# Performance work log

Measured on AMD Instinct MI355X. Metric: run time of the kernel, lower is better.

The kernel has to match this reference:

```python
import jax, jax.numpy as jnp
import numpy as np

D_MODEL = 1024
H = 16
D_HEAD = D_MODEL // H


def setup_inputs() -> dict:
    key = jax.random.key(0)
    ks = jax.random.split(key, 9)
    B, S = 2, 2048
    x = jax.random.normal(ks[0], (B, S, D_MODEL), dtype=jnp.float32)
    s = 1.0 / np.sqrt(D_HEAD)
    # per-head Q/K/V linears, stacked: W[h, out, in], b[h, out] (torch Linear: y = x W^T + b)
    Wq = jax.random.normal(ks[1], (H, D_HEAD, D_HEAD), dtype=jnp.float32) * s
    bq = jax.random.normal(ks[2], (H, D_HEAD), dtype=jnp.float32) * 0.01
    Wk = jax.random.normal(ks[3], (H, D_HEAD, D_HEAD), dtype=jnp.float32) * s
    bk = jax.random.normal(ks[4], (H, D_HEAD), dtype=jnp.float32) * 0.01
    Wv = jax.random.normal(ks[5], (H, D_HEAD, D_HEAD), dtype=jnp.float32) * s
    bv = jax.random.normal(ks[6], (H, D_HEAD), dtype=jnp.float32) * 0.01
    Wo = jax.random.normal(ks[7], (D_MODEL, D_MODEL), dtype=jnp.float32) / np.sqrt(D_MODEL)
    bo = jax.random.normal(ks[8], (D_MODEL,), dtype=jnp.float32) * 0.01
    return {"x": x, "Wq": Wq, "bq": bq, "Wk": Wk, "bk": bk,
            "Wv": Wv, "bv": bv, "Wo": Wo, "bo": bo}


def reference(x, Wq, bq, Wk, bk, Wv, bv, Wo, bo):
    B, S, D = x.shape
    xh = x.reshape(B, S, H, D_HEAD)  # split along feature dim, head-major
    q = jnp.einsum('bshi,hoi->bsho', xh, Wq) + bq
    k = jnp.einsum('bshi,hoi->bsho', xh, Wk) + bk
    v = jnp.einsum('bshi,hoi->bsho', xh, Wv) + bv
    scale = 1.0 / jnp.sqrt(jnp.asarray(D_HEAD, dtype=x.dtype))  # source scales by sqrt(d_model//h)
    scores = jnp.einsum('bqhd,bkhd->bhqk', q, k) * scale
    causal = jnp.tril(jnp.ones((S, S), dtype=bool))
    scores = jnp.where(causal, scores, -jnp.inf)
    attn = jax.nn.softmax(scores, axis=-1)
    out = jnp.einsum('bhqk,bkhd->bqhd', attn, v).reshape(B, S, D)
    return out @ Wo.T + bo
```

## Files before the change

kernel.cpp:

```cpp
#include <hip/hip_runtime.h>
#include <cstddef>

#define Bc 2
#define Sc 2048
#define Dc 1024
#define Hc 16
#define QSC 0.18033688011112042f

typedef short short8 __attribute__((ext_vector_type(8)));
typedef float floatx4 __attribute__((ext_vector_type(4)));
typedef unsigned short ushort_t;

#if __has_builtin(__builtin_amdgcn_exp2f)
#define EXP2F(x) __builtin_amdgcn_exp2f(x)
#else
#define EXP2F(x) exp2f(x)
#endif

__device__ __forceinline__ unsigned pack2bf(float a, float b) {
    unsigned ua = __float_as_uint(a) + 0x8000u;
    unsigned ub = __float_as_uint(b) + 0x8000u;
    return __builtin_amdgcn_perm(ub, ua, 0x07060302u);
}
__device__ __forceinline__ ushort_t f2bf(float f) {
    return (ushort_t)((__float_as_uint(f) + 0x8000u) >> 16);
}

template<int N>
__device__ __forceinline__ float row_ror(float x) {
    return __int_as_float(__builtin_amdgcn_update_dpp(
        0, __float_as_int(x), 0x120 + N, 0xF, 0xF, false));
}
__device__ __forceinline__ float rsum16(float x) {
    x += row_ror<1>(x); x += row_ror<2>(x);
    x += row_ror<4>(x); x += row_ror<8>(x);
    return x;
}

__global__ __launch_bounds__(256) void wcvt_kernel(
    const float* __restrict__ Wo, const float* __restrict__ Wq,
    const float* __restrict__ Wk, const float* __restrict__ Wv,
    ushort_t* __restrict__ WoB, ushort_t* __restrict__ Wqkvb)
{
    int idx = (blockIdx.x * 256 + threadIdx.x) * 8;
    const float* src; ushort_t* dst;
    if (idx < 1048576) { src = Wo + idx; dst = WoB + idx; }
    else {
        int r = idx - 1048576;
        int w = r >> 16, off = r & 65535;
        src = (w == 0 ? Wq : (w == 1 ? Wk : Wv)) + off;
        dst = Wqkvb + r;
    }
    float4 a = *(const float4*)src;
    float4 c = *(const float4*)(src + 4);
    uint4 o;
    o.x = pack2bf(a.x, a.y); o.y = pack2bf(a.z, a.w);
    o.z = pack2bf(c.x, c.y); o.w = pack2bf(c.z, c.w);
    *(uint4*)dst = o;
}

__global__ __launch_bounds__(256) void qkv_kernel(
    const float* __restrict__ x, const ushort_t* __restrict__ Wqkvb,
    const float* __restrict__ bq, const float* __restrict__ bk, const float* __restrict__ bv,
    ushort_t* __restrict__ Qb, ushort_t* __restrict__ Kb, ushort_t* __restrict__ VT)
{
    const int blk = blockIdx.x;
    const int st = blk & 31, h = (blk >> 5) & 15, b = blk >> 9;
    const int bh = b * Hc + h, s0 = st * 64;
    const int tid = threadIdx.x, wid = tid >> 6, lane = tid & 63;
    const int lr = lane & 15, quad = lane >> 4;

    __shared__ ushort_t Xs[64 * 72];
    __shared__ ushort_t Wsh[3 * 64 * 72];

    {
        int row = tid >> 2, cg = tid & 3;
        const float* xp = x + ((size_t)(b * Sc + s0 + row)) * Dc + h * 64 + cg * 16;
        float4 v0 = *(const float4*)xp;
        float4 v1 = *(const float4*)(xp + 4);
        float4 v2 = *(const float4*)(xp + 8);
        float4 v3 = *(const float4*)(xp + 12);
        uint4 p0, p1;
        p0.x = pack2bf(v0.x, v0.y); p0.y = pack2bf(v0.z, v0.w);
        p0.z = pack2bf(v1.x, v1.y); p0.w = pack2bf(v1.z, v1.w);
        p1.x = pack2bf(v2.x, v2.y); p1.y = pack2bf(v2.z, v2.w);
        p1.z = pack2bf(v3.x, v3.y); p1.w = pack2bf(v3.z, v3.w);
        *(uint4*)(Xs + row * 72 + cg * 16) = p0;
        *(uint4*)(Xs + row * 72 + cg * 16 + 8) = p1;
    }
    {
        const ushort_t* Wg = Wqkvb + (size_t)h * 4096;
#pragma unroll
        for (int s = 0; s < 6; ++s) {
            int c = tid + s * 256;
            int w = c >> 9, rem = c & 511, row = rem >> 3, part = rem & 7;
            *(short8*)(Wsh + (w * 64 + row) * 72 + part * 8) =
                *(const short8*)(Wg + (size_t)w * 65536 + row * 64 + part * 8);
        }
    }
    __syncthreads();

    short8 af0 = *(const short8*)(Xs + (wid * 16 + lr) * 72 + quad * 8);
    short8 af1 = *(const short8*)(Xs + (wid * 16 + lr) * 72 + 32 + quad * 8);

    const float* bias3[3] = {bq + h * 64, bk + h * 64, bv + h * 64};
    const int row = tid >> 2, cg = tid & 3;

#pragma unroll
    for (int w = 0; w < 3; ++w) {
        ushort_t* Ot = Wsh + w * 64 * 72;
        short8 bf0[4], bf1[4];
#pragma unroll
        for (int n = 0; n < 4; ++n) {
            const ushort_t* wrow = Ot + (n * 16 + lr) * 72;
            bf0[n] = *(const short8*)(wrow + quad * 8);
            bf1[n] = *(const short8*)(wrow + 32 + quad * 8);
        }
        floatx4 acc[4];
#pragma unroll
        for (int n = 0; n < 4; ++n) {
            floatx4 z = {0.f, 0.f, 0.f, 0.f};
            acc[n] = __builtin_amdgcn_mfma_f32_16x16x32_bf16(af0, bf0[n], z, 0, 0, 0);
            acc[n] = __builtin_amdgcn_mfma_f32_16x16x32_bf16(af1, bf1[n], acc[n], 0, 0, 0);
        }
        __syncthreads();
        if (w < 2) {
#pragma unroll
            for (int n = 0; n < 4; ++n) {
                float bias = bias3[w][n * 16 + lr];
#pragma unroll
                for (int r = 0; r < 4; ++r) {
                    float val = acc[n][r] + bias;
                    if (w == 0) val *= QSC;
                    Ot[(wid * 16 + quad * 4 + r) * 72 + n * 16 + lr] = f2bf(val);
                }
            }
        } else {
#pragma unroll
            for (int n = 0; n < 4; ++n) {
                float bias = bias3[2][n * 16 + lr];
                uint2 pw;
                pw.x = pack2bf(acc[n][0] + bias, acc[n][1] + bias);
                pw.y = pack2bf(acc[n][2] + bias, acc[n][3] + bias);
                *(uint2*)(Ot + (n * 16 + lr) * 72 + wid * 16 + quad * 4) = pw;
            }
        }
        __syncthreads();
        const ushort_t* srcp = Ot + row * 72 + cg * 16;
        uint4 d0 = *(const uint4*)srcp;
        uint4 d1 = *(const uint4*)(srcp + 8);
        ushort_t* dst;
        if (w == 0)      dst = Qb + ((size_t)bh * Sc + s0 + row) * 64 + cg * 16;
        else if (w == 1) dst = Kb + ((size_t)bh * Sc + s0 + row) * 64 + cg * 16;
        else             dst = VT + ((size_t)bh * 64 + row) * Sc + s0 + cg * 16;
        *(uint4*)dst = d0;
        *(uint4*)(dst + 8) = d1;
    }
}

#define ST 88

__global__ __launch_bounds__(256, 2) void attn_kernel(
    const ushort_t* __restrict__ Qg, const ushort_t* __restrict__ Kg,
    const ushort_t* __restrict__ VTg, ushort_t* __restrict__ Actx)
{
    const int blk = blockIdx.x;
    const int tpair = blk & 15;
    const int bh = blk >> 4;
    const int b = bh >> 4, h = bh & 15;
    const int qta = 31 - tpair, qtb = tpair;
    const int s0a = qta * 64, s0b = qtb * 64;
    const int tid = threadIdx.x, wid = tid >> 6, lane = tid & 63;
    const int lr = lane & 15, quad = lane >> 4;

    __shared__ ushort_t Ks[64 * ST];
    __shared__ ushort_t Vs[64 * ST];
    __shared__ ushort_t Ps[8 * 16 * ST];

    const ushort_t* Kbh = Kg + (size_t)bh * Sc * 64;
    const ushort_t* Vbh = VTg + (size_t)bh * 64 * Sc;

    const ushort_t* QrA = Qg + ((size_t)bh * Sc + s0a + wid * 16 + lr) * 64;
    const ushort_t* QrB = Qg + ((size_t)bh * Sc + s0b + wid * 16 + lr) * 64;
    short8 qfa0 = *(const short8*)(QrA + quad * 8);
    short8 qfa1 = *(const short8*)(QrA + 32 + quad * 8);
    short8 qfb0 = *(const short8*)(QrB + quad * 8);
    short8 qfb1 = *(const short8*)(QrB + 32 + quad * 8);

    floatx4 oA[4], oB[4];
    float lA[4], lB[4];
#pragma unroll
    for (int n = 0; n < 4; ++n) { oA[n] = floatx4{0,0,0,0}; oB[n] = floatx4{0,0,0,0}; }
#pragma unroll
    for (int r = 0; r < 4; ++r) { lA[r] = 0.f; lB[r] = 0.f; }

    const int sr0 = tid >> 3, sp0 = tid & 7;
    const int sr1 = sr0 + 32, sp1 = sp0;

    short8 kr0 = *(const short8*)(Kbh + (size_t)sr0 * 64 + sp0 * 8);
    short8 kr1 = *(const short8*)(Kbh + (size_t)sr1 * 64 + sp1 * 8);
    short8 vr0 = *(const short8*)(Vbh + (size_t)sr0 * Sc + sp0 * 8);
    short8 vr1 = *(const short8*)(Vbh + (size_t)sr1 * Sc + sp1 * 8);
    *(short8*)(Ks + sr0 * ST + sp0 * 8) = kr0;
    *(short8*)(Ks + sr1 * ST + sp1 * 8) = kr1;
    *(short8*)(Vs + sr0 * ST + sp0 * 8) = vr0;
    *(short8*)(Vs + sr1 * ST + sp1 * 8) = vr1;
    __syncthreads();

    ushort_t* PwA = Ps + wid * 16 * ST;
    ushort_t* PwB = Ps + (4 + wid) * 16 * ST;

    for (int kt = 0; kt <= qta; ++kt) {
        const bool hasB = (kt <= qtb);

        short8 kf[4][2], vf[4][2];
#pragma unroll
        for (int kg = 0; kg < 4; ++kg) {
            const ushort_t* kp = Ks + (4 * lr + kg) * ST;
            kf[kg][0] = *(const short8*)(kp + quad * 8);
            kf[kg][1] = *(const short8*)(kp + 32 + quad * 8);
        }
#pragma unroll
        for (int n = 0; n < 4; ++n) {
            const ushort_t* vp = Vs + (n * 16 + lr) * ST;
            vf[n][0] = *(const short8*)(vp + quad * 8);
            vf[n][1] = *(const short8*)(vp + 32 + quad * 8);
        }

        if (kt < qta) {
            const ushort_t* kn = Kbh + (size_t)(kt + 1) * 64 * 64;
            const ushort_t* vn = Vbh + (kt + 1) * 64;
            kr0 = *(const short8*)(kn + (size_t)sr0 * 64 + sp0 * 8);
            kr1 = *(const short8*)(kn + (size_t)sr1 * 64 + sp1 * 8);
            vr0 = *(const short8*)(vn + (size_t)sr0 * Sc + sp0 * 8);
            vr1 = *(const short8*)(vn + (size_t)sr1 * Sc + sp1 * 8);
        }

        floatx4 sA[4], sB[4];
#pragma unroll
        for (int kg = 0; kg < 4; ++kg) {
            floatx4 z = {0.f, 0.f, 0.f, 0.f};
            floatx4 t0 = __builtin_amdgcn_mfma_f32_16x16x32_bf16(qfa0, kf[kg][0], z, 0, 0, 0);
            sA[kg] = __builtin_amdgcn_mfma_f32_16x16x32_bf16(qfa1, kf[kg][1], t0, 0, 0, 0);
        }
        if (hasB) {
#pragma unroll
            for (int kg = 0; kg < 4; ++kg) {
                floatx4 z = {0.f, 0.f, 0.f, 0.f};
                floatx4 t0 = __builtin_amdgcn_mfma_f32_16x16x32_bf16(qfb0, kf[kg][0], z, 0, 0, 0);
                sB[kg] = __builtin_amdgcn_mfma_f32_16x16x32_bf16(qfb1, kf[kg][1], t0, 0, 0, 0);
            }
        }

        if (kt == qta) {
#pragma unroll
            for (int kg = 0; kg < 4; ++kg) {
                int key = 4 * lr + kg;
#pragma unroll
                for (int r = 0; r < 4; ++r)
                    if (key > wid * 16 + quad * 4 + r) sA[kg][r] = -1e30f;
            }
        }
        if (hasB && kt == qtb) {
#pragma unroll
            for (int kg = 0; kg < 4; ++kg) {
                int key = 4 * lr + kg;
#pragma unroll
                for (int r = 0; r < 4; ++r)
                    if (key > wid * 16 + quad * 4 + r) sB[kg][r] = -1e30f;
            }
        }

#pragma unroll
        for (int r = 0; r < 4; ++r) {
            float p0 = EXP2F(sA[0][r]), p1 = EXP2F(sA[1][r]);
            float p2 = EXP2F(sA[2][r]), p3 = EXP2F(sA[3][r]);
            lA[r] += rsum16(p0 + p1 + p2 + p3);
            uint2 pw; pw.x = pack2bf(p0, p1); pw.y = pack2bf(p2, p3);
            *(uint2*)(PwA + (quad * 4 + r) * ST + 4 * lr) = pw;
        }
        if (hasB) {
#pragma unroll
            for (int r = 0; r < 4; ++r) {
                float p0 = EXP2F(sB[0][r]), p1 = EXP2F(sB[1][r]);
                float p2 = EXP2F(sB[2][r]), p3 = EXP2F(sB[3][r]);
                lB[r] += rsum16(p0 + p1 + p2 + p3);
                uint2 pw; pw.x = pack2bf(p0, p1); pw.y = pack2bf(p2, p3);
                *(uint2*)(PwB + (quad * 4 + r) * ST + 4 * lr) = pw;
            }
        }

        short8 pa0 = *(const short8*)(PwA + lr * ST + quad * 8);
        short8 pa1 = *(const short8*)(PwA + lr * ST + 32 + quad * 8);
#pragma unroll
        for (int n = 0; n < 4; ++n) {
            oA[n] = __builtin_amdgcn_mfma_f32_16x16x32_bf16(pa0, vf[n][0], oA[n], 0, 0, 0);
            oA[n] = __builtin_amdgcn_mfma_f32_16x16x32_bf16(pa1, vf[n][1], oA[n], 0, 0, 0);
        }
        if (hasB) {
            short8 pb0 = *(const short8*)(PwB + lr * ST + quad * 8);
            short8 pb1 = *(const short8*)(PwB + lr * ST + 32 + quad * 8);
#pragma unroll
            for (int n = 0; n < 4; ++n) {
                oB[n] = __builtin_amdgcn_mfma_f32_16x16x32_bf16(pb0, vf[n][0], oB[n], 0, 0, 0);
                oB[n] = __builtin_amdgcn_mfma_f32_16x16x32_bf16(pb1, vf[n][1], oB[n], 0, 0, 0);
            }
        }

        __syncthreads();
        if (kt < qta) {
            *(short8*)(Ks + sr0 * ST + sp0 * 8) = kr0;
            *(short8*)(Ks + sr1 * ST + sp1 * 8) = kr1;
            *(short8*)(Vs + sr0 * ST + sp0 * 8) = vr0;
            *(short8*)(Vs + sr1 * ST + sp1 * 8) = vr1;
            __syncthreads();
        }
    }

#pragma unroll
    for (int r = 0; r < 4; ++r) {
        float invA = 1.f / lA[r], invB = 1.f / lB[r];
        int rowA = s0a + wid * 16 + quad * 4 + r;
        int rowB = s0b + wid * 16 + quad * 4 + r;
        ushort_t* dA = Actx + ((size_t)(b * Sc + rowA)) * Dc + h * 64 + lr;
        ushort_t* dB = Actx + ((size_t)(b * Sc + rowB)) * Dc + h * 64 + lr;
#pragma unroll
        for (int n = 0; n < 4; ++n) {
            dA[n * 16] = f2bf(oA[n][r] * invA);
            dB[n * 16] = f2bf(oB[n][r] * invB);
        }
    }
}

__global__ __launch_bounds__(256, 2) void proj_kernel(
    const ushort_t* __restrict__ Ab, const ushort_t* __restrict__ Wb,
    const float* __restrict__ bo, float* __restrict__ out)
{
    const int bn = blockIdx.x & 15, bm = blockIdx.x >> 4;
    const int tid = threadIdx.x, wid = tid >> 6, lane = tid & 63;
    const int lr = lane & 15, quad = lane >> 4;
    const int wm = wid * 32;

    __shared__ ushort_t As[128 * 40];
    __shared__ ushort_t Bs[64 * 40];

    floatx4 acc[2][4];
#pragma unroll
    for (int i = 0; i < 2; ++i)
#pragma unroll
        for (int n = 0; n < 4; ++n) acc[i][n] = floatx4{0.f, 0.f, 0.f, 0.f};

    const ushort_t* Ag = Ab + (size_t)bm * 128 * 1024;
    const ushort_t* Wg = Wb + (size_t)bn * 64 * 1024;

    const int ar0 = tid >> 2, ap0 = tid & 3;
    const int ar1 = ar0 + 64;

    short8 a0 = *(const short8*)(Ag + (size_t)ar0 * 1024 + ap0 * 8);
    short8 a1 = *(const short8*)(Ag + (size_t)ar1 * 1024 + ap0 * 8);
    short8 b0 = *(const short8*)(Wg + (size_t)ar0 * 1024 + ap0 * 8);
    *(short8*)(As + ar0 * 40 + ap0 * 8) = a0;
    *(short8*)(As + ar1 * 40 + ap0 * 8) = a1;
    *(short8*)(Bs + ar0 * 40 + ap0 * 8) = b0;
    __syncthreads();

    for (int k0 = 0; k0 < 1024; k0 += 32) {
        short8 fa0 = *(const short8*)(As + (wm + lr) * 40 + quad * 8);
        short8 fa1 = *(const short8*)(As + (wm + 16 + lr) * 40 + quad * 8);
        short8 fb[4];
#pragma unroll
        for (int n = 0; n < 4; ++n)
            fb[n] = *(const short8*)(Bs + (n * 16 + lr) * 40 + quad * 8);

        if (k0 < 992) {
            int k1 = k0 + 32;
            a0 = *(const short8*)(Ag + (size_t)ar0 * 1024 + k1 + ap0 * 8);
            a1 = *(const short8*)(Ag + (size_t)ar1 * 1024 + k1 + ap0 * 8);
            b0 = *(const short8*)(Wg + (size_t)ar0 * 1024 + k1 + ap0 * 8);
        }
#pragma unroll
        for (int n = 0; n < 4; ++n) {
            acc[0][n] = __builtin_amdgcn_mfma_f32_16x16x32_bf16(fa0, fb[n], acc[0][n], 0, 0, 0);
            acc[1][n] = __builtin_amdgcn_mfma_f32_16x16x32_bf16(fa1, fb[n], acc[1][n], 0, 0, 0);
        }
        __syncthreads();
        if (k0 < 992) {
            *(short8*)(As + ar0 * 40 + ap0 * 8) = a0;
            *(short8*)(As + ar1 * 40 + ap0 * 8) = a1;
            *(short8*)(Bs + ar0 * 40 + ap0 * 8) = b0;
            __syncthreads();
        }
    }

#pragma unroll
    for (int i = 0; i < 2; ++i) {
        int mrow = bm * 128 + wm + i * 16 + quad * 4;
#pragma unroll
        for (int n = 0; n < 4; ++n) {
            int col = bn * 64 + n * 16 + lr;
            float bias = bo[col];
#pragma unroll
            for (int r = 0; r < 4; ++r)
                out[(size_t)(mrow + r) * 1024 + col] = acc[i][n][r] + bias;
        }
    }
}

extern "C" void kernel_launch(void* const* d_in, const int* in_sizes, int n_in,
                              void* d_out, int out_size, void* d_ws, size_t ws_size,
                              hipStream_t stream)
{
    (void)in_sizes; (void)n_in; (void)out_size; (void)ws_size;
    const float* x  = (const float*)d_in[0];
    const float* Wq = (const float*)d_in[1];
    const float* bq = (const float*)d_in[2];
    const float* Wk = (const float*)d_in[3];
    const float* bk = (const float*)d_in[4];
    const float* Wv = (const float*)d_in[5];
    const float* bv = (const float*)d_in[6];
    const float* Wo = (const float*)d_in[7];
    const float* bo = (const float*)d_in[8];
    float* out = (float*)d_out;

    const size_t N4 = (size_t)Bc * Hc * Sc * 64;
    ushort_t* base  = (ushort_t*)d_ws;
    ushort_t* Qb    = base;
    ushort_t* Kb    = base + N4;
    ushort_t* VT    = base + 2 * N4;
    ushort_t* Actx  = base + 3 * N4;
    ushort_t* WoB   = base + 4 * N4;
    ushort_t* Wqkvb = base + 4 * N4 + 1048576;

    wcvt_kernel<<<dim3(608), dim3(256), 0, stream>>>(Wo, Wq, Wk, Wv, WoB, Wqkvb);
    qkv_kernel<<<dim3(Bc * Hc * (Sc / 64)), dim3(256), 0, stream>>>(
        x, Wqkvb, bq, bk, bv, Qb, Kb, VT);
    attn_kernel<<<dim3(Bc * Hc * 16), dim3(256), 0, stream>>>(Qb, Kb, VT, Actx);
    proj_kernel<<<dim3(32 * 16), dim3(256), 0, stream>>>(Actx, WoB, bo, out);
}
```

Baseline: 152.4 us.

## Halve attention block to two waves each handling two query sub-tiles

The attention kernel now runs 128 threads per block, and each wave processes two 16-row query groups. K fragments loaded from LDS are reused across twice as many MFMAs and the per-block LDS staging cost is spread over more work per wave. The block-to-(head, tile-pair) mapping is reordered so the first and second half of the grid get complementary tile pairs, and the LDS row stride shrinks from 88 to 72. Register pressure rises from the doubled accumulators, and there are fewer waves to hide latency.

```diff
diff --git a/kernel.cpp b/kernel.cpp
--- a/kernel.cpp
+++ b/kernel.cpp
@@ -158,15 +158,17 @@
     }
 }
 
-#define ST 88
-
-__global__ __launch_bounds__(256, 2) void attn_kernel(
+#define ST 72
+
+__global__ __launch_bounds__(128) void attn_kernel(
     const ushort_t* __restrict__ Qg, const ushort_t* __restrict__ Kg,
     const ushort_t* __restrict__ VTg, ushort_t* __restrict__ Actx)
 {
     const int blk = blockIdx.x;
-    const int tpair = blk & 15;
-    const int bh = blk >> 4;
+    const int u = blk & 255;
+    const int bh = u & 31;
+    const int f = (u >> 5) & 7;
+    const int tpair = (blk < 256) ? f : 15 - f;
     const int b = bh >> 4, h = bh & 15;
     const int qta = 31 - tpair, qtb = tpair;
     const int s0a = qta * 64, s0b = qtb * 64;
@@ -180,46 +182,124 @@
     const ushort_t* Kbh = Kg + (size_t)bh * Sc * 64;
     const ushort_t* Vbh = VTg + (size_t)bh * 64 * Sc;
 
-    const ushort_t* QrA = Qg + ((size_t)bh * Sc + s0a + wid * 16 + lr) * 64;
-    const ushort_t* QrB = Qg + ((size_t)bh * Sc + s0b + wid * 16 + lr) * 64;
-    short8 qfa0 = *(const short8*)(QrA + quad * 8);
-    short8 qfa1 = *(const short8*)(QrA + 32 + quad * 8);
-    short8 qfb0 = *(const short8*)(QrB + quad * 8);
-    short8 qfb1 = *(const short8*)(QrB + 32 + quad * 8);
-
-    floatx4 oA[4], oB[4];
-    float lA[4], lB[4];
-#pragma unroll
-    for (int n = 0; n < 4; ++n) { oA[n] = floatx4{0,0,0,0}; oB[n] = floatx4{0,0,0,0}; }
-#pragma unroll
-    for (int r = 0; r < 4; ++r) { lA[r] = 0.f; lB[r] = 0.f; }
-
-    const int sr0 = tid >> 3, sp0 = tid & 7;
-    const int sr1 = sr0 + 32, sp1 = sp0;
-
-    short8 kr0 = *(const short8*)(Kbh + (size_t)sr0 * 64 + sp0 * 8);
-    short8 kr1 = *(const short8*)(Kbh + (size_t)sr1 * 64 + sp1 * 8);
-    short8 vr0 = *(const short8*)(Vbh + (size_t)sr0 * Sc + sp0 * 8);
-    short8 vr1 = *(const short8*)(Vbh + (size_t)sr1 * Sc + sp1 * 8);
-    *(short8*)(Ks + sr0 * ST + sp0 * 8) = kr0;
-    *(short8*)(Ks + sr1 * ST + sp1 * 8) = kr1;
-    *(short8*)(Vs + sr0 * ST + sp0 * 8) = vr0;
-    *(short8*)(Vs + sr1 * ST + sp1 * 8) = vr1;
+    short8 qa[2][2], qb[2][2];
+#pragma unroll
+    for (int g = 0; g < 2; ++g) {
+        const ushort_t* QrA = Qg + ((size_t)bh * Sc + s0a + wid * 32 + g * 16 + lr) * 64;
+        const ushort_t* QrB = Qg + ((size_t)bh * Sc + s0b + wid * 32 + g * 16 + lr) * 64;
+        qa[g][0] = *(const short8*)(QrA + quad * 8);
+        qa[g][1] = *(const short8*)(QrA + 32 + quad * 8);
+        qb[g][0] = *(const short8*)(QrB + quad * 8);
+        qb[g][1] = *(const short8*)(QrB + 32 + quad * 8);
+    }
+
+    floatx4 oA[2][4], oB[2][4];
+    float lA[2][4], lB[2][4];
+#pragma unroll
+    for (int g = 0; g < 2; ++g)
+#pragma unroll
+        for (int n = 0; n < 4; ++n) { oA[g][n] = floatx4{0,0,0,0}; oB[g][n] = floatx4{0,0,0,0}; }
+#pragma unroll
+    for (int g = 0; g < 2; ++g)
+#pragma unroll
+        for (int r = 0; r < 4; ++r) { lA[g][r] = 0.f; lB[g][r] = 0.f; }
+
+    const int sr = tid >> 3, sp = tid & 7;
+
+    short8 kr[4], vr[4];
+#pragma unroll
+    for (int s = 0; s < 4; ++s) {
+        kr[s] = *(const short8*)(Kbh + (size_t)(sr + s * 16) * 64 + sp * 8);
+        vr[s] = *(const short8*)(Vbh + (size_t)(sr + s * 16) * Sc + sp * 8);
+    }
+#pragma unroll
+    for (int s = 0; s < 4; ++s) {
+        *(short8*)(Ks + (sr + s * 16) * ST + sp * 8) = kr[s];
+        *(short8*)(Vs + (sr + s * 16) * ST + sp * 8) = vr[s];
+    }
     __syncthreads();
-
-    ushort_t* PwA = Ps + wid * 16 * ST;
-    ushort_t* PwB = Ps + (4 + wid) * 16 * ST;
 
     for (int kt = 0; kt <= qta; ++kt) {
         const bool hasB = (kt <= qtb);
 
-        short8 kf[4][2], vf[4][2];
+        short8 kf[4][2];
 #pragma unroll
         for (int kg = 0; kg < 4; ++kg) {
             const ushort_t* kp = Ks + (4 * lr + kg) * ST;
             kf[kg][0] = *(const short8*)(kp + quad * 8);
             kf[kg][1] = *(const short8*)(kp + 32 + quad * 8);
         }
+
+        if (kt < qta) {
+            const ushort_t* kn = Kbh + (size_t)(kt + 1) * 4096;
+            const ushort_t* vn = Vbh + (kt + 1) * 64;
+#pragma unroll
+            for (int s = 0; s < 4; ++s) {
+                kr[s] = *(const short8*)(kn + (size_t)(sr + s * 16) * 64 + sp * 8);
+                vr[s] = *(const short8*)(vn + (size_t)(sr + s * 16) * Sc + sp * 8);
+            }
+        }
+
+#pragma unroll
+        for (int g = 0; g < 2; ++g) {
+            floatx4 s4[4];
+#pragma unroll
+            for (int kg = 0; kg < 4; ++kg) {
+                floatx4 z = {0.f, 0.f, 0.f, 0.f};
+                floatx4 t0 = __builtin_amdgcn_mfma_f32_16x16x32_bf16(qa[g][0], kf[kg][0], z, 0, 0, 0);
+                s4[kg] = __builtin_amdgcn_mfma_f32_16x16x32_bf16(qa[g][1], kf[kg][1], t0, 0, 0, 0);
+            }
+            if (kt == qta) {
+#pragma unroll
+                for (int kg = 0; kg < 4; ++kg) {
+                    int key = 4 * lr + kg;
+#pragma unroll
+                    for (int r = 0; r < 4; ++r)
+                        if (key > wid * 32 + g * 16 + quad * 4 + r) s4[kg][r] = -1e30f;
+                }
+            }
+            ushort_t* Pg = Ps + ((wid * 2 + g) * 16) * ST;
+#pragma unroll
+            for (int r = 0; r < 4; ++r) {
+                float p0 = EXP2F(s4[0][r]), p1 = EXP2F(s4[1][r]);
+                float p2 = EXP2F(s4[2][r]), p3 = EXP2F(s4[3][r]);
+                lA[g][r] += rsum16(p0 + p1 + p2 + p3);
+                uint2 pw; pw.x = pack2bf(p0, p1); pw.y = pack2bf(p2, p3);
+                *(uint2*)(Pg + (quad * 4 + r) * ST + 4 * lr) = pw;
+            }
+        }
+        if (hasB) {
+#pragma unroll
+            for (int g = 0; g < 2; ++g) {
+                floatx4 s4[4];
+#pragma unroll
+                for (int kg = 0; kg < 4; ++kg) {
+                    floatx4 z = {0.f, 0.f, 0.f, 0.f};
+                    floatx4 t0 = __builtin_amdgcn_mfma_f32_16x16x32_bf16(qb[g][0], kf[kg][0], z, 0, 0, 0);
+                    s4[kg] = __builtin_amdgcn_mfma_f32_16x16x32_bf16(qb[g][1], kf[kg][1], t0, 0, 0, 0);
+                }
+                if (kt == qtb) {
+#pragma unroll
+                    for (int kg = 0; kg < 4; ++kg) {
+                        int key = 4 * lr + kg;
+#pragma unroll
+                        for (int r = 0; r < 4; ++r)
+                            if (key > wid * 32 + g * 16 + quad * 4 + r) s4[kg][r] = -1e30f;
+                    }
+                }
+                ushort_t* Pg = Ps + (((2 + wid) * 2 + g) * 16) * ST;
+#pragma unroll
+                for (int r = 0; r < 4; ++r) {
+                    float p0 = EXP2F(s4[0][r]), p1 = EXP2F(s4[1][r]);
+                    float p2 = EXP2F(s4[2][r]), p3 = EXP2F(s4[3][r]);
+                    lB[g][r] += rsum16(p0 + p1 + p2 + p3);
+                    uint2 pw; pw.x = pack2bf(p0, p1); pw.y = pack2bf(p2, p3);
+                    *(uint2*)(Pg + (quad * 4 + r) * ST + 4 * lr) = pw;
+                }
+            }
+        }
+
+        short8 vf[4][2];
 #pragma unroll
         for (int n = 0; n < 4; ++n) {
             const ushort_t* vp = Vs + (n * 16 + lr) * ST;
@@ -227,107 +307,56 @@
             vf[n][1] = *(const short8*)(vp + 32 + quad * 8);
         }
 
-        if (kt < qta) {
-            const ushort_t* kn = Kbh + (size_t)(kt + 1) * 64 * 64;
-            const ushort_t* vn = Vbh + (kt + 1) * 64;
-            kr0 = *(const short8*)(kn + (size_t)sr0 * 64 + sp0 * 8);
-            kr1 = *(const short8*)(kn + (size_t)sr1 * 64 + sp1 * 8);
-            vr0 = *(const short8*)(vn + (size_t)sr0 * Sc + sp0 * 8);
-            vr1 = *(const short8*)(vn + (size_t)sr1 * Sc + sp1 * 8);
-        }
-
-        floatx4 sA[4], sB[4];
-#pragma unroll
-        for (int kg = 0; kg < 4; ++kg) {
-            floatx4 z = {0.f, 0.f, 0.f, 0.f};
-            floatx4 t0 = __builtin_amdgcn_mfma_f32_16x16x32_bf16(qfa0, kf[kg][0], z, 0, 0, 0);
-            sA[kg] = __builtin_amdgcn_mfma_f32_16x16x32_bf16(qfa1, kf[kg][1], t0, 0, 0, 0);
+#pragma unroll
+        for (int g = 0; g < 2; ++g) {
+            const ushort_t* Pg = Ps + ((wid * 2 + g) * 16) * ST;
+            short8 pf0 = *(const short8*)(Pg + lr * ST + quad * 8);
+            short8 pf1 = *(const short8*)(Pg + lr * ST + 32 + quad * 8);
+#pragma unroll
+            for (int n = 0; n < 4; ++n) {
+                oA[g][n] = __builtin_amdgcn_mfma_f32_16x16x32_bf16(pf0, vf[n][0], oA[g][n], 0, 0, 0);
+                oA[g][n] = __builtin_amdgcn_mfma_f32_16x16x32_bf16(pf1, vf[n][1], oA[g][n], 0, 0, 0);
+            }
         }
         if (hasB) {
 #pragma unroll
-            for (int kg = 0; kg < 4; ++kg) {
-                floatx4 z = {0.f, 0.f, 0.f, 0.f};
-                floatx4 t0 = __builtin_amdgcn_mfma_f32_16x16x32_bf16(qfb0, kf[kg][0], z, 0, 0, 0);
-                sB[kg] = __builtin_amdgcn_mfma_f32_16x16x32_bf16(qfb1, kf[kg][1], t0, 0, 0, 0);
-            }
-        }
-
-        if (kt == qta) {
-#pragma unroll
-            for (int kg = 0; kg < 4; ++kg) {
-                int key = 4 * lr + kg;
-#pragma unroll
-                for (int r = 0; r < 4; ++r)
-                    if (key > wid * 16 + quad * 4 + r) sA[kg][r] = -1e30f;
-            }
-        }
-        if (hasB && kt == qtb) {
-#pragma unroll
-            for (int kg = 0; kg < 4; ++kg) {
-                int key = 4 * lr + kg;
-#pragma unroll
-                for (int r = 0; r < 4; ++r)
-                    if (key > wid * 16 + quad * 4 + r) sB[kg][r] = -1e30f;
-            }
-        }
-
-#pragma unroll
-        for (int r = 0; r < 4; ++r) {
-            float p0 = EXP2F(sA[0][r]), p1 = EXP2F(sA[1][r]);
-            float p2 = EXP2F(sA[2][r]), p3 = EXP2F(sA[3][r]);
-            lA[r] += rsum16(p0 + p1 + p2 + p3);
-            uint2 pw; pw.x = pack2bf(p0, p1); pw.y = pack2bf(p2, p3);
-            *(uint2*)(PwA + (quad * 4 + r) * ST + 4 * lr) = pw;
-        }
-        if (hasB) {
-#pragma unroll
-            for (int r = 0; r < 4; ++r) {
-                float p0 = EXP2F(sB[0][r]), p1 = EXP2F(sB[1][r]);
-                float p2 = EXP2F(sB[2][r]), p3 = EXP2F(sB[3][r]);
-                lB[r] += rsum16(p0 + p1 + p2 + p3);
-                uint2 pw; pw.x = pack2bf(p0, p1); pw.y = pack2bf(p2, p3);
-                *(uint2*)(PwB + (quad * 4 + r) * ST + 4 * lr) = pw;
-            }
-        }
-
-        short8 pa0 = *(const short8*)(PwA + lr * ST + quad * 8);
-        short8 pa1 = *(const short8*)(PwA + lr * ST + 32 + quad * 8);
-#pragma unroll
-        for (int n = 0; n < 4; ++n) {
-            oA[n] = __builtin_amdgcn_mfma_f32_16x16x32_bf16(pa0, vf[n][0], oA[n], 0, 0, 0);
-            oA[n] = __builtin_amdgcn_mfma_f32_16x16x32_bf16(pa1, vf[n][1], oA[n], 0, 0, 0);
-        }
-        if (hasB) {
-            short8 pb0 = *(const short8*)(PwB + lr * ST + quad * 8);
-            short8 pb1 = *(const short8*)(PwB + lr * ST + 32 + quad * 8);
-#pragma unroll
-            for (int n = 0; n < 4; ++n) {
-                oB[n] = __builtin_amdgcn_mfma_f32_16x16x32_bf16(pb0, vf[n][0], oB[n], 0, 0, 0);
-                oB[n] = __builtin_amdgcn_mfma_f32_16x16x32_bf16(pb1, vf[n][1], oB[n], 0, 0, 0);
+            for (int g = 0; g < 2; ++g) {
+                const ushort_t* Pg = Ps + (((2 + wid) * 2 + g) * 16) * ST;
+                short8 pf0 = *(const short8*)(Pg + lr * ST + quad * 8);
+                short8 pf1 = *(const short8*)(Pg + lr * ST + 32 + quad * 8);
+#pragma unroll
+                for (int n = 0; n < 4; ++n) {
+                    oB[g][n] = __builtin_amdgcn_mfma_f32_16x16x32_bf16(pf0, vf[n][0], oB[g][n], 0, 0, 0);
+                    oB[g][n] = __builtin_amdgcn_mfma_f32_16x16x32_bf16(pf1, vf[n][1], oB[g][n], 0, 0, 0);
+                }
             }
         }
 
         __syncthreads();
         if (kt < qta) {
-            *(short8*)(Ks + sr0 * ST + sp0 * 8) = kr0;
-            *(short8*)(Ks + sr1 * ST + sp1 * 8) = kr1;
-            *(short8*)(Vs + sr0 * ST + sp0 * 8) = vr0;
-            *(short8*)(Vs + sr1 * ST + sp1 * 8) = vr1;
+#pragma unroll
+            for (int s = 0; s < 4; ++s) {
+                *(short8*)(Ks + (sr + s * 16) * ST + sp * 8) = kr[s];
+                *(short8*)(Vs + (sr + s * 16) * ST + sp * 8) = vr[s];
+            }
             __syncthreads();
         }
     }
 
 #pragma unroll
-    for (int r = 0; r < 4; ++r) {
-        float invA = 1.f / lA[r], invB = 1.f / lB[r];
-        int rowA = s0a + wid * 16 + quad * 4 + r;
-        int rowB = s0b + wid * 16 + quad * 4 + r;
-        ushort_t* dA = Actx + ((size_t)(b * Sc + rowA)) * Dc + h * 64 + lr;
-        ushort_t* dB = Actx + ((size_t)(b * Sc + rowB)) * Dc + h * 64 + lr;
-#pragma unroll
-        for (int n = 0; n < 4; ++n) {
-            dA[n * 16] = f2bf(oA[n][r] * invA);
-            dB[n * 16] = f2bf(oB[n][r] * invB);
+    for (int g = 0; g < 2; ++g) {
+#pragma unroll
+        for (int r = 0; r < 4; ++r) {
+            float invA = 1.f / lA[g][r], invB = 1.f / lB[g][r];
+            int rowA = s0a + wid * 32 + g * 16 + quad * 4 + r;
+            int rowB = s0b + wid * 32 + g * 16 + quad * 4 + r;
+            ushort_t* dA = Actx + ((size_t)(b * Sc + rowA)) * Dc + h * 64 + lr;
+            ushort_t* dB = Actx + ((size_t)(b * Sc + rowB)) * Dc + h * 64 + lr;
+#pragma unroll
+            for (int n = 0; n < 4; ++n) {
+                dA[n * 16] = f2bf(oA[g][n][r] * invA);
+                dB[n * 16] = f2bf(oB[g][n][r] * invB);
+            }
         }
     }
 }
@@ -434,6 +463,6 @@
     wcvt_kernel<<<dim3(608), dim3(256), 0, stream>>>(Wo, Wq, Wk, Wv, WoB, Wqkvb);
     qkv_kernel<<<dim3(Bc * Hc * (Sc / 64)), dim3(256), 0, stream>>>(
         x, Wqkvb, bq, bk, bv, Qb, Kb, VT);
-    attn_kernel<<<dim3(Bc * Hc * 16), dim3(256), 0, stream>>>(Qb, Kb, VT, Actx);
+    attn_kernel<<<dim3(512), dim3(128), 0, stream>>>(Qb, Kb, VT, Actx);
     proj_kernel<<<dim3(32 * 16), dim3(256), 0, stream>>>(Actx, WoB, bo, out);
 }
```

Result: slower. 170.2 us (+11.6%).

## Double-buffer K/V tiles in attention, remap block order, shrink LDS stride

Applied to the files above, without the earlier changes.

The attention kernel now keeps two shared-memory buffers for K and V, so the next tile is stored into the idle buffer and each iteration needs one barrier instead of two. The block index is remapped so consecutive blocks cover different batch-head pairs and the two launch halves take mirrored tile pairs, which spreads work across CUs more evenly. The LDS row stride drops from 88 to 72 to keep total shared memory similar after doubling the buffers, which may change bank-conflict behaviour on the fragment reads.

```diff
diff --git a/kernel.cpp b/kernel.cpp
--- a/kernel.cpp
+++ b/kernel.cpp
@@ -158,23 +158,25 @@
     }
 }
 
-#define ST 88
+#define ST 72
 
 __global__ __launch_bounds__(256, 2) void attn_kernel(
     const ushort_t* __restrict__ Qg, const ushort_t* __restrict__ Kg,
     const ushort_t* __restrict__ VTg, ushort_t* __restrict__ Actx)
 {
     const int blk = blockIdx.x;
-    const int tpair = blk & 15;
-    const int bh = blk >> 4;
+    const int u = blk & 255;
+    const int bh = u & 31;
+    const int f = (u >> 5) & 7;
+    const int tpair = (blk < 256) ? f : 15 - f;
     const int b = bh >> 4, h = bh & 15;
     const int qta = 31 - tpair, qtb = tpair;
     const int s0a = qta * 64, s0b = qtb * 64;
     const int tid = threadIdx.x, wid = tid >> 6, lane = tid & 63;
     const int lr = lane & 15, quad = lane >> 4;
 
-    __shared__ ushort_t Ks[64 * ST];
-    __shared__ ushort_t Vs[64 * ST];
+    __shared__ ushort_t Ks[2][64 * ST];
+    __shared__ ushort_t Vs[2][64 * ST];
     __shared__ ushort_t Ps[8 * 16 * ST];
 
     const ushort_t* Kbh = Kg + (size_t)bh * Sc * 64;
@@ -195,45 +197,48 @@
     for (int r = 0; r < 4; ++r) { lA[r] = 0.f; lB[r] = 0.f; }
 
     const int sr0 = tid >> 3, sp0 = tid & 7;
-    const int sr1 = sr0 + 32, sp1 = sp0;
+    const int sr1 = sr0 + 32;
 
     short8 kr0 = *(const short8*)(Kbh + (size_t)sr0 * 64 + sp0 * 8);
-    short8 kr1 = *(const short8*)(Kbh + (size_t)sr1 * 64 + sp1 * 8);
+    short8 kr1 = *(const short8*)(Kbh + (size_t)sr1 * 64 + sp0 * 8);
     short8 vr0 = *(const short8*)(Vbh + (size_t)sr0 * Sc + sp0 * 8);
-    short8 vr1 = *(const short8*)(Vbh + (size_t)sr1 * Sc + sp1 * 8);
-    *(short8*)(Ks + sr0 * ST + sp0 * 8) = kr0;
-    *(short8*)(Ks + sr1 * ST + sp1 * 8) = kr1;
-    *(short8*)(Vs + sr0 * ST + sp0 * 8) = vr0;
-    *(short8*)(Vs + sr1 * ST + sp1 * 8) = vr1;
+    short8 vr1 = *(const short8*)(Vbh + (size_t)sr1 * Sc + sp0 * 8);
+    *(short8*)(Ks[0] + sr0 * ST + sp0 * 8) = kr0;
+    *(short8*)(Ks[0] + sr1 * ST + sp0 * 8) = kr1;
+    *(short8*)(Vs[0] + sr0 * ST + sp0 * 8) = vr0;
+    *(short8*)(Vs[0] + sr1 * ST + sp0 * 8) = vr1;
     __syncthreads();
 
     ushort_t* PwA = Ps + wid * 16 * ST;
     ushort_t* PwB = Ps + (4 + wid) * 16 * ST;
 
+    int buf = 0;
     for (int kt = 0; kt <= qta; ++kt) {
         const bool hasB = (kt <= qtb);
+        const ushort_t* Kc = Ks[buf];
+        const ushort_t* Vc = Vs[buf];
 
         short8 kf[4][2], vf[4][2];
 #pragma unroll
         for (int kg = 0; kg < 4; ++kg) {
-            const ushort_t* kp = Ks + (4 * lr + kg) * ST;
+            const ushort_t* kp = Kc + (4 * lr + kg) * ST;
             kf[kg][0] = *(const short8*)(kp + quad * 8);
             kf[kg][1] = *(const short8*)(kp + 32 + quad * 8);
         }
 #pragma unroll
         for (int n = 0; n < 4; ++n) {
-            const ushort_t* vp = Vs + (n * 16 + lr) * ST;
+            const ushort_t* vp = Vc + (n * 16 + lr) * ST;
             vf[n][0] = *(const short8*)(vp + quad * 8);
             vf[n][1] = *(const short8*)(vp + 32 + quad * 8);
         }
 
         if (kt < qta) {
-            const ushort_t* kn = Kbh + (size_t)(kt + 1) * 64 * 64;
+            const ushort_t* kn = Kbh + (size_t)(kt + 1) * 4096;
             const ushort_t* vn = Vbh + (kt + 1) * 64;
             kr0 = *(const short8*)(kn + (size_t)sr0 * 64 + sp0 * 8);
-            kr1 = *(const short8*)(kn + (size_t)sr1 * 64 + sp1 * 8);
+            kr1 = *(const short8*)(kn + (size_t)sr1 * 64 + sp0 * 8);
             vr0 = *(const short8*)(vn + (size_t)sr0 * Sc + sp0 * 8);
-            vr1 = *(const short8*)(vn + (size_t)sr1 * Sc + sp1 * 8);
+            vr1 = *(const short8*)(vn + (size_t)sr1 * Sc + sp0 * 8);
         }
 
         floatx4 sA[4], sB[4];
@@ -307,14 +312,14 @@
             }
         }
 
+        if (kt < qta) {
+            *(short8*)(Ks[buf ^ 1] + sr0 * ST + sp0 * 8) = kr0;
+            *(short8*)(Ks[buf ^ 1] + sr1 * ST + sp0 * 8) = kr1;
+            *(short8*)(Vs[buf ^ 1] + sr0 * ST + sp0 * 8) = vr0;
+            *(short8*)(Vs[buf ^ 1] + sr1 * ST + sp0 * 8) = vr1;
+            buf ^= 1;
+        }
         __syncthreads();
-        if (kt < qta) {
-            *(short8*)(Ks + sr0 * ST + sp0 * 8) = kr0;
-            *(short8*)(Ks + sr1 * ST + sp1 * 8) = kr1;
-            *(short8*)(Vs + sr0 * ST + sp0 * 8) = vr0;
-            *(short8*)(Vs + sr1 * ST + sp1 * 8) = vr1;
-            __syncthreads();
-        }
     }
 
 #pragma unroll
@@ -434,6 +439,6 @@
     wcvt_kernel<<<dim3(608), dim3(256), 0, stream>>>(Wo, Wq, Wk, Wv, WoB, Wqkvb);
     qkv_kernel<<<dim3(Bc * Hc * (Sc / 64)), dim3(256), 0, stream>>>(
         x, Wqkvb, bq, bk, bv, Qb, Kb, VT);
-    attn_kernel<<<dim3(Bc * Hc * 16), dim3(256), 0, stream>>>(Qb, Kb, VT, Actx);
+    attn_kernel<<<dim3(512), dim3(256), 0, stream>>>(Qb, Kb, VT, Actx);
     proj_kernel<<<dim3(32 * 16), dim3(256), 0, stream>>>(Actx, WoB, bo, out);
 }
```

Measured after the change: 146.8 us. 1.04x faster.

## Drop LDS staging in attention and projection, load MFMA fragments from global

Applied to the files above, without the earlier changes.

The attention kernel stops pairing a long and a short query tile per block. It launches one block per query tile (1024 blocks) in an interleaved order, and each wave reads its K and V fragments straight from global memory instead of a shared-memory tile. The projection GEMM likewise drops its LDS double buffer and loads A and W fragments directly. Both changes remove block-wide barriers and LDS traffic and raise occupancy hints. In exchange, reuse of K/V and weights across waves now depends on the caches, and global-load latency is no longer hidden by explicit prefetch.

```diff
diff --git a/kernel.cpp b/kernel.cpp
--- a/kernel.cpp
+++ b/kernel.cpp
@@ -158,181 +158,107 @@
     }
 }
 
-#define ST 88
-
-__global__ __launch_bounds__(256, 2) void attn_kernel(
+#define ST 72
+
+__global__ __launch_bounds__(256, 3) void attn_kernel(
     const ushort_t* __restrict__ Qg, const ushort_t* __restrict__ Kg,
     const ushort_t* __restrict__ VTg, ushort_t* __restrict__ Actx)
 {
     const int blk = blockIdx.x;
-    const int tpair = blk & 15;
-    const int bh = blk >> 4;
+    const int bh = blk & 31;
+    const int idx = blk >> 5;
+    const int g = idx & 7, m = idx >> 3;
+    const int qt = (m == 0) ? g : (m == 1) ? 15 - g : (m == 2) ? 16 + g : 31 - g;
+    const int s0 = qt * 64;
     const int b = bh >> 4, h = bh & 15;
-    const int qta = 31 - tpair, qtb = tpair;
-    const int s0a = qta * 64, s0b = qtb * 64;
     const int tid = threadIdx.x, wid = tid >> 6, lane = tid & 63;
     const int lr = lane & 15, quad = lane >> 4;
 
-    __shared__ ushort_t Ks[64 * ST];
-    __shared__ ushort_t Vs[64 * ST];
-    __shared__ ushort_t Ps[8 * 16 * ST];
+    __shared__ ushort_t Ps[4 * 16 * ST];
 
     const ushort_t* Kbh = Kg + (size_t)bh * Sc * 64;
     const ushort_t* Vbh = VTg + (size_t)bh * 64 * Sc;
 
-    const ushort_t* QrA = Qg + ((size_t)bh * Sc + s0a + wid * 16 + lr) * 64;
-    const ushort_t* QrB = Qg + ((size_t)bh * Sc + s0b + wid * 16 + lr) * 64;
-    short8 qfa0 = *(const short8*)(QrA + quad * 8);
-    short8 qfa1 = *(const short8*)(QrA + 32 + quad * 8);
-    short8 qfb0 = *(const short8*)(QrB + quad * 8);
-    short8 qfb1 = *(const short8*)(QrB + 32 + quad * 8);
-
-    floatx4 oA[4], oB[4];
-    float lA[4], lB[4];
-#pragma unroll
-    for (int n = 0; n < 4; ++n) { oA[n] = floatx4{0,0,0,0}; oB[n] = floatx4{0,0,0,0}; }
-#pragma unroll
-    for (int r = 0; r < 4; ++r) { lA[r] = 0.f; lB[r] = 0.f; }
-
-    const int sr0 = tid >> 3, sp0 = tid & 7;
-    const int sr1 = sr0 + 32, sp1 = sp0;
-
-    short8 kr0 = *(const short8*)(Kbh + (size_t)sr0 * 64 + sp0 * 8);
-    short8 kr1 = *(const short8*)(Kbh + (size_t)sr1 * 64 + sp1 * 8);
-    short8 vr0 = *(const short8*)(Vbh + (size_t)sr0 * Sc + sp0 * 8);
-    short8 vr1 = *(const short8*)(Vbh + (size_t)sr1 * Sc + sp1 * 8);
-    *(short8*)(Ks + sr0 * ST + sp0 * 8) = kr0;
-    *(short8*)(Ks + sr1 * ST + sp1 * 8) = kr1;
-    *(short8*)(Vs + sr0 * ST + sp0 * 8) = vr0;
-    *(short8*)(Vs + sr1 * ST + sp1 * 8) = vr1;
-    __syncthreads();
-
-    ushort_t* PwA = Ps + wid * 16 * ST;
-    ushort_t* PwB = Ps + (4 + wid) * 16 * ST;
-
-    for (int kt = 0; kt <= qta; ++kt) {
-        const bool hasB = (kt <= qtb);
-
-        short8 kf[4][2], vf[4][2];
+    const ushort_t* Qr = Qg + ((size_t)bh * Sc + s0 + wid * 16 + lr) * 64;
+    short8 qf0 = *(const short8*)(Qr + quad * 8);
+    short8 qf1 = *(const short8*)(Qr + 32 + quad * 8);
+
+    floatx4 o[4];
+    float l[4];
+#pragma unroll
+    for (int n = 0; n < 4; ++n) o[n] = floatx4{0.f, 0.f, 0.f, 0.f};
+#pragma unroll
+    for (int r = 0; r < 4; ++r) l[r] = 0.f;
+
+    ushort_t* Pw = Ps + wid * 16 * ST;
+
+    const ushort_t* kp = Kbh + (size_t)(4 * lr) * 64 + quad * 8;
+    const ushort_t* vp = Vbh + (size_t)lr * Sc + quad * 8;
+
+    for (int kt = 0; kt <= qt; ++kt) {
+        short8 kf[4][2];
 #pragma unroll
         for (int kg = 0; kg < 4; ++kg) {
-            const ushort_t* kp = Ks + (4 * lr + kg) * ST;
-            kf[kg][0] = *(const short8*)(kp + quad * 8);
-            kf[kg][1] = *(const short8*)(kp + 32 + quad * 8);
-        }
-#pragma unroll
-        for (int n = 0; n < 4; ++n) {
-            const ushort_t* vp = Vs + (n * 16 + lr) * ST;
-            vf[n][0] = *(const short8*)(vp + quad * 8);
-            vf[n][1] = *(const short8*)(vp + 32 + quad * 8);
-        }
-
-        if (kt < qta) {
-            const ushort_t* kn = Kbh + (size_t)(kt + 1) * 64 * 64;
-            const ushort_t* vn = Vbh + (kt + 1) * 64;
-            kr0 = *(const short8*)(kn + (size_t)sr0 * 64 + sp0 * 8);
-            kr1 = *(const short8*)(kn + (size_t)sr1 * 64 + sp1 * 8);
-            vr0 = *(const short8*)(vn + (size_t)sr0 * Sc + sp0 * 8);
-            vr1 = *(const short8*)(vn + (size_t)sr1 * Sc + sp1 * 8);
-        }
-
-        floatx4 sA[4], sB[4];
+            const ushort_t* kpp = kp + (size_t)kt * 4096 + kg * 64;
+            kf[kg][0] = *(const short8*)(kpp);
+            kf[kg][1] = *(const short8*)(kpp + 32);
+        }
+        short8 vf[4][2];
+#pragma unroll
+        for (int n = 0; n < 4; ++n) {
+            const ushort_t* vpp = vp + (size_t)n * 16 * Sc + kt * 64;
+            vf[n][0] = *(const short8*)(vpp);
+            vf[n][1] = *(const short8*)(vpp + 32);
+        }
+
+        floatx4 s4[4];
 #pragma unroll
         for (int kg = 0; kg < 4; ++kg) {
             floatx4 z = {0.f, 0.f, 0.f, 0.f};
-            floatx4 t0 = __builtin_amdgcn_mfma_f32_16x16x32_bf16(qfa0, kf[kg][0], z, 0, 0, 0);
-            sA[kg] = __builtin_amdgcn_mfma_f32_16x16x32_bf16(qfa1, kf[kg][1], t0, 0, 0, 0);
-        }
-        if (hasB) {
-#pragma unroll
-            for (int kg = 0; kg < 4; ++kg) {
-                floatx4 z = {0.f, 0.f, 0.f, 0.f};
-                floatx4 t0 = __builtin_amdgcn_mfma_f32_16x16x32_bf16(qfb0, kf[kg][0], z, 0, 0, 0);
-                sB[kg] = __builtin_amdgcn_mfma_f32_16x16x32_bf16(qfb1, kf[kg][1], t0, 0, 0, 0);
-            }
-        }
-
-        if (kt == qta) {
+            floatx4 t0 = __builtin_amdgcn_mfma_f32_16x16x32_bf16(qf0, kf[kg][0], z, 0, 0, 0);
+            s4[kg] = __builtin_amdgcn_mfma_f32_16x16x32_bf16(qf1, kf[kg][1], t0, 0, 0, 0);
+        }
+
+        if (kt == qt) {
 #pragma unroll
             for (int kg = 0; kg < 4; ++kg) {
                 int key = 4 * lr + kg;
 #pragma unroll
                 for (int r = 0; r < 4; ++r)
-                    if (key > wid * 16 + quad * 4 + r) sA[kg][r] = -1e30f;
+                    if (key > wid * 16 + quad * 4 + r) s4[kg][r] = -1e30f;
             }
         }
-        if (hasB && kt == qtb) {
-#pragma unroll
-            for (int kg = 0; kg < 4; ++kg) {
-                int key = 4 * lr + kg;
-#pragma unroll
-                for (int r = 0; r < 4; ++r)
-                    if (key > wid * 16 + quad * 4 + r) sB[kg][r] = -1e30f;
-            }
-        }
 
 #pragma unroll
         for (int r = 0; r < 4; ++r) {
-            float p0 = EXP2F(sA[0][r]), p1 = EXP2F(sA[1][r]);
-            float p2 = EXP2F(sA[2][r]), p3 = EXP2F(sA[3][r]);
-            lA[r] += rsum16(p0 + p1 + p2 + p3);
+            float p0 = EXP2F(s4[0][r]), p1 = EXP2F(s4[1][r]);
+            float p2 = EXP2F(s4[2][r]), p3 = EXP2F(s4[3][r]);
+            l[r] += rsum16(p0 + p1 + p2 + p3);
             uint2 pw; pw.x = pack2bf(p0, p1); pw.y = pack2bf(p2, p3);
-            *(uint2*)(PwA + (quad * 4 + r) * ST + 4 * lr) = pw;
-        }
-        if (hasB) {
-#pragma unroll
-            for (int r = 0; r < 4; ++r) {
-                float p0 = EXP2F(sB[0][r]), p1 = EXP2F(sB[1][r]);
-                float p2 = EXP2F(sB[2][r]), p3 = EXP2F(sB[3][r]);
-                lB[r] += rsum16(p0 + p1 + p2 + p3);
-                uint2 pw; pw.x = pack2bf(p0, p1); pw.y = pack2bf(p2, p3);
-                *(uint2*)(PwB + (quad * 4 + r) * ST + 4 * lr) = pw;
-            }
-        }
-
-        short8 pa0 = *(const short8*)(PwA + lr * ST + quad * 8);
-        short8 pa1 = *(const short8*)(PwA + lr * ST + 32 + quad * 8);
-#pragma unroll
-        for (int n = 0; n < 4; ++n) {
-            oA[n] = __builtin_amdgcn_mfma_f32_16x16x32_bf16(pa0, vf[n][0], oA[n], 0, 0, 0);
-            oA[n] = __builtin_amdgcn_mfma_f32_16x16x32_bf16(pa1, vf[n][1], oA[n], 0, 0, 0);
-        }
-        if (hasB) {
-            short8 pb0 = *(const short8*)(PwB + lr * ST + quad * 8);
-            short8 pb1 = *(const short8*)(PwB + lr * ST + 32 + quad * 8);
-#pragma unroll
-            for (int n = 0; n < 4; ++n) {
-                oB[n] = __builtin_amdgcn_mfma_f32_16x16x32_bf16(pb0, vf[n][0], oB[n], 0, 0, 0);
-                oB[n] = __builtin_amdgcn_mfma_f32_16x16x32_bf16(pb1, vf[n][1], oB[n], 0, 0, 0);
-            }
-        }
-
-        __syncthreads();
-        if (kt < qta) {
-            *(short8*)(Ks + sr0 * ST + sp0 * 8) = kr0;
-            *(short8*)(Ks + sr1 * ST + sp1 * 8) = kr1;
-            *(short8*)(Vs + sr0 * ST + sp0 * 8) = vr0;
-            *(short8*)(Vs + sr1 * ST + sp1 * 8) = vr1;
-            __syncthreads();
+            *(uint2*)(Pw + (quad * 4 + r) * ST + 4 * lr) = pw;
+        }
+
+        short8 pf0 = *(const short8*)(Pw + lr * ST + quad * 8);
+        short8 pf1 = *(const short8*)(Pw + lr * ST + 32 + quad * 8);
+#pragma unroll
+        for (int n = 0; n < 4; ++n) {
+            o[n] = __builtin_amdgcn_mfma_f32_16x16x32_bf16(pf0, vf[n][0], o[n], 0, 0, 0);
+            o[n] = __builtin_amdgcn_mfma_f32_16x16x32_bf16(pf1, vf[n][1], o[n], 0, 0, 0);
         }
     }
 
 #pragma unroll
     for (int r = 0; r < 4; ++r) {
-        float invA = 1.f / lA[r], invB = 1.f / lB[r];
-        int rowA = s0a + wid * 16 + quad * 4 + r;
-        int rowB = s0b + wid * 16 + quad * 4 + r;
-        ushort_t* dA = Actx + ((size_t)(b * Sc + rowA)) * Dc + h * 64 + lr;
-        ushort_t* dB = Actx + ((size_t)(b * Sc + rowB)) * Dc + h * 64 + lr;
-#pragma unroll
-        for (int n = 0; n < 4; ++n) {
-            dA[n * 16] = f2bf(oA[n][r] * invA);
-            dB[n * 16] = f2bf(oB[n][r] * invB);
-        }
-    }
-}
-
-__global__ __launch_bounds__(256, 2) void proj_kernel(
+        float inv = 1.f / l[r];
+        int srow = s0 + wid * 16 + quad * 4 + r;
+        ushort_t* d = Actx + ((size_t)(b * Sc + srow)) * Dc + h * 64 + lr;
+#pragma unroll
+        for (int n = 0; n < 4; ++n)
+            d[n * 16] = f2bf(o[n][r] * inv);
+    }
+}
+
+__global__ __launch_bounds__(256, 4) void proj_kernel(
     const ushort_t* __restrict__ Ab, const ushort_t* __restrict__ Wb,
     const float* __restrict__ bo, float* __restrict__ out)
 {
@@ -341,54 +267,27 @@
     const int lr = lane & 15, quad = lane >> 4;
     const int wm = wid * 32;
 
-    __shared__ ushort_t As[128 * 40];
-    __shared__ ushort_t Bs[64 * 40];
-
     floatx4 acc[2][4];
 #pragma unroll
     for (int i = 0; i < 2; ++i)
 #pragma unroll
         for (int n = 0; n < 4; ++n) acc[i][n] = floatx4{0.f, 0.f, 0.f, 0.f};
 
-    const ushort_t* Ag = Ab + (size_t)bm * 128 * 1024;
-    const ushort_t* Wg = Wb + (size_t)bn * 64 * 1024;
-
-    const int ar0 = tid >> 2, ap0 = tid & 3;
-    const int ar1 = ar0 + 64;
-
-    short8 a0 = *(const short8*)(Ag + (size_t)ar0 * 1024 + ap0 * 8);
-    short8 a1 = *(const short8*)(Ag + (size_t)ar1 * 1024 + ap0 * 8);
-    short8 b0 = *(const short8*)(Wg + (size_t)ar0 * 1024 + ap0 * 8);
-    *(short8*)(As + ar0 * 40 + ap0 * 8) = a0;
-    *(short8*)(As + ar1 * 40 + ap0 * 8) = a1;
-    *(short8*)(Bs + ar0 * 40 + ap0 * 8) = b0;
-    __syncthreads();
+    const ushort_t* Ag0 = Ab + (size_t)(bm * 128 + wm + lr) * 1024 + quad * 8;
+    const ushort_t* Ag1 = Ag0 + (size_t)16 * 1024;
+    const ushort_t* Wg  = Wb + (size_t)(bn * 64 + lr) * 1024 + quad * 8;
 
     for (int k0 = 0; k0 < 1024; k0 += 32) {
-        short8 fa0 = *(const short8*)(As + (wm + lr) * 40 + quad * 8);
-        short8 fa1 = *(const short8*)(As + (wm + 16 + lr) * 40 + quad * 8);
+        short8 fa0 = *(const short8*)(Ag0 + k0);
+        short8 fa1 = *(const short8*)(Ag1 + k0);
         short8 fb[4];
 #pragma unroll
         for (int n = 0; n < 4; ++n)
-            fb[n] = *(const short8*)(Bs + (n * 16 + lr) * 40 + quad * 8);
-
-        if (k0 < 992) {
-            int k1 = k0 + 32;
-            a0 = *(const short8*)(Ag + (size_t)ar0 * 1024 + k1 + ap0 * 8);
-            a1 = *(const short8*)(Ag + (size_t)ar1 * 1024 + k1 + ap0 * 8);
-            b0 = *(const short8*)(Wg + (size_t)ar0 * 1024 + k1 + ap0 * 8);
-        }
+            fb[n] = *(const short8*)(Wg + (size_t)n * 16 * 1024 + k0);
 #pragma unroll
         for (int n = 0; n < 4; ++n) {
             acc[0][n] = __builtin_amdgcn_mfma_f32_16x16x32_bf16(fa0, fb[n], acc[0][n], 0, 0, 0);
             acc[1][n] = __builtin_amdgcn_mfma_f32_16x16x32_bf16(fa1, fb[n], acc[1][n], 0, 0, 0);
-        }
-        __syncthreads();
-        if (k0 < 992) {
-            *(short8*)(As + ar0 * 40 + ap0 * 8) = a0;
-            *(short8*)(As + ar1 * 40 + ap0 * 8) = a1;
-            *(short8*)(Bs + ar0 * 40 + ap0 * 8) = b0;
-            __syncthreads();
         }
     }
 
@@ -434,6 +333,6 @@
     wcvt_kernel<<<dim3(608), dim3(256), 0, stream>>>(Wo, Wq, Wk, Wv, WoB, Wqkvb);
     qkv_kernel<<<dim3(Bc * Hc * (Sc / 64)), dim3(256), 0, stream>>>(
         x, Wqkvb, bq, bk, bv, Qb, Kb, VT);
-    attn_kernel<<<dim3(Bc * Hc * 16), dim3(256), 0, stream>>>(Qb, Kb, VT, Actx);
+    attn_kernel<<<dim3(1024), dim3(256), 0, stream>>>(Qb, Kb, VT, Actx);
     proj_kernel<<<dim3(32 * 16), dim3(256), 0, stream>>>(Actx, WoB, bo, out);
 }
```

After: 257.8 us. +69.1%, slower.
